# Optimization experiments

Measured on AMD Instinct MI355X. Metric: run time of the kernel, lower is better.

The kernel has to match this reference:

```python
import jax, jax.numpy as jnp
import numpy as np

N_BITS = 14
L = 1 << N_BITS
B, C_IN, C_OUT = 32, 32, 64

def _neigh_idx():
    # (L, n_bits): index j flipped at bit b -> j ^ (1<<b)
    s = jnp.arange(L)
    return jnp.stack([s ^ (1 << b) for b in range(N_BITS)], axis=1)

def setup_inputs() -> dict:
    key = jax.random.key(0)
    k1, k2, k3, k4 = jax.random.split(key, 4)
    x = jax.random.normal(k1, (B, C_IN, L), dtype=jnp.float32)
    w_self = jnp.ones((), dtype=jnp.float32)
    w_bits = jax.random.normal(k2, (N_BITS,), dtype=jnp.float32) * 0.1
    # Conv1d(kernel_size=1) weight squeezed to (C_out, C_in)
    mix_w = jax.random.normal(k3, (C_OUT, C_IN), dtype=jnp.float32) * (1.0 / np.sqrt(C_IN))
    mix_b = jax.random.normal(k4, (C_OUT,), dtype=jnp.float32) * 0.01
    return {"x": x, "w_self": w_self, "w_bits": w_bits, "mix_w": mix_w, "mix_b": mix_b}

def reference(x, w_self, w_bits, mix_w, mix_b):
    n_bits = w_bits.shape[0]
    idx = _neigh_idx()                          # (L, n_bits), int32
    xn = x[:, :, idx]                           # (B, C, L, n_bits) XOR-neighbor gather
    neigh_sum = jnp.einsum('bclk,k->bcl', xn, w_bits)
    y = w_self * x + neigh_sum
    y = y / (1.0 + n_bits)                      # agg == 'mean'
    # 1x1 conv mix: (B,C,L) x (C_out,C_in) -> (B,C_out,L)
    return jnp.einsum('bcl,oc->bol', y, mix_w) + mix_b[None, :, None]
```

## Files before the change

kernel.cpp:

```cpp
#include <hip/hip_runtime.h>

#define TILE  256
#define CIN   32
#define COUT  64
#define LSIZE 16384
#define NBITS 14

typedef float f32x4 __attribute__((ext_vector_type(4)));

__device__ __forceinline__ f32x4 splat4(float s) {
    f32x4 v = {s, s, s, s};
    return v;
}

__global__ __launch_bounds__(256, 5)
void hamming_fused(const float* __restrict__ x,
                   const float* __restrict__ w_self,
                   const float* __restrict__ w_bits,
                   const float* __restrict__ mix_w,
                   const float* __restrict__ mix_b,
                   float* __restrict__ out)
{
    __shared__ float xs[CIN][TILE];

    const int tid  = threadIdx.x;
    const int lane = tid & 63;
    const int wv   = tid >> 6;

    const int d    = blockIdx.x;
    const int xcd  = d & 7;
    const int j    = d >> 3;
    const int b    = xcd * 4 + (j >> 6);
    const int tile = j & 63;
    const int base = tile * TILE;
    const float* xb = x + (size_t)b * CIN * LSIZE;

    #pragma unroll
    for (int i = 0; i < 8; ++i) {
        const int r = wv + i * 4;
        const float* src = xb + (size_t)r * LSIZE + base + lane * 4;
        __builtin_amdgcn_global_load_lds(
            (const __attribute__((address_space(1))) void*)src,
            (__attribute__((address_space(3))) void*)&xs[r][lane * 4],
            16, 0, 0);
    }

    const float ws = w_self[0];
    float wb[NBITS];
    #pragma unroll
    for (int k = 0; k < NBITS; ++k) wb[k] = w_bits[k];

    __syncthreads();

    const int c0ch = wv * 8;
    const int colb = lane * 4;

    f32x4 yv[8];
    #pragma unroll
    for (int cc = 0; cc < 8; cc += 2) {
        f32x4 pf[2][6];
        #pragma unroll
        for (int u = 0; u < 2; ++u) {
            const float* xr = xb + (size_t)(c0ch + cc + u) * LSIZE;
            #pragma unroll
            for (int kk = 0; kk < 6; ++kk)
                pf[u][kk] = *(const f32x4*)(xr + ((base ^ (TILE << kk)) + colb));
        }
        #pragma unroll
        for (int u = 0; u < 2; ++u) {
            const int c = c0ch + cc + u;
            const f32x4 s = *(const f32x4*)&xs[c][colb];
            f32x4 a = s * ws;
            a.x += wb[0] * s.y; a.y += wb[0] * s.x; a.z += wb[0] * s.w; a.w += wb[0] * s.z;
            a.x += wb[1] * s.z; a.y += wb[1] * s.w; a.z += wb[1] * s.x; a.w += wb[1] * s.y;
            #pragma unroll
            for (int k = 2; k < 8; ++k) {
                const f32x4 t = *(const f32x4*)&xs[c][colb ^ (1 << k)];
                a += wb[k] * t;
            }
            #pragma unroll
            for (int kk = 0; kk < 6; ++kk)
                a += wb[8 + kk] * pf[u][kk];
            yv[cc + u] = a * (1.0f / 15.0f);
        }
    }
    __syncthreads();

    #pragma unroll
    for (int cc = 0; cc < 8; ++cc)
        *(f32x4*)&xs[c0ch + cc][colb] = yv[cc];
    __syncthreads();

    const int tx  = tid & 63;
    const int ty  = tid >> 6;
    const int cb2 = tx << 2;
    const int o0  = ty * 16;

    f32x4 acc[16];
    #pragma unroll
    for (int q = 0; q < 4; ++q) {
        const f32x4 b4 = *(const f32x4*)(mix_b + o0 + q * 4);
        acc[q * 4 + 0] = splat4(b4.x);
        acc[q * 4 + 1] = splat4(b4.y);
        acc[q * 4 + 2] = splat4(b4.z);
        acc[q * 4 + 3] = splat4(b4.w);
    }

    #pragma unroll 1
    for (int c0 = 0; c0 < CIN; c0 += 4) {
        const f32x4 y0 = *(const f32x4*)&xs[c0 + 0][cb2];
        const f32x4 y1 = *(const f32x4*)&xs[c0 + 1][cb2];
        const f32x4 y2 = *(const f32x4*)&xs[c0 + 2][cb2];
        const f32x4 y3 = *(const f32x4*)&xs[c0 + 3][cb2];
        const float* wp = mix_w + o0 * CIN + c0;
        #pragma unroll
        for (int jj = 0; jj < 16; ++jj) {
            const f32x4 w4 = *(const f32x4*)(wp + jj * CIN);
            acc[jj] += w4.x * y0;
            acc[jj] += w4.y * y1;
            acc[jj] += w4.z * y2;
            acc[jj] += w4.w * y3;
        }
    }

    float* ob = out + (size_t)b * COUT * LSIZE;
    #pragma unroll
    for (int jj = 0; jj < 16; ++jj) {
        f32x4* p = (f32x4*)(ob + (size_t)(o0 + jj) * LSIZE + base + cb2);
        __builtin_nontemporal_store(acc[jj], p);
    }
}

extern "C" void kernel_launch(void* const* d_in, const int* in_sizes, int n_in,
                              void* d_out, int out_size, void* d_ws, size_t ws_size,
                              hipStream_t stream) {
    const float* x      = (const float*)d_in[0];
    const float* w_self = (const float*)d_in[1];
    const float* w_bits = (const float*)d_in[2];
    const float* mix_w  = (const float*)d_in[3];
    const float* mix_b  = (const float*)d_in[4];
    float* out = (float*)d_out;

    hamming_fused<<<dim3(2048), 256, 0, stream>>>(x, w_self, w_bits, mix_w, mix_b, out);
}
```

Baseline: 232.9 us.

## Stage mix weights in LDS and software-pipeline neighbor prefetch across channels

Loads the 64x32 mix weight matrix into shared memory with async global-to-LDS copies, so the channel-mix loop reads weights from LDS instead of issuing scalar or global loads. The far-neighbor global prefetches become a rolling 3-slot pipeline issued two channels ahead, with the first two started before the LDS tile load. Results are written straight back into the shared tile, which drops one barrier and the yv register array. The mix loop is unrolled by 2 and the occupancy hint is lowered from 5 to 4 to allow more registers, at the cost of 8 KB extra LDS per block and possibly fewer resident waves.

Result: faster. 216.1 us (-7.2%).

```diff
diff --git a/kernel.cpp b/kernel.cpp
--- a/kernel.cpp
+++ b/kernel.cpp
@@ -13,7 +13,7 @@
     return v;
 }
 
-__global__ __launch_bounds__(256, 5)
+__global__ __launch_bounds__(256, 4)
 void hamming_fused(const float* __restrict__ x,
                    const float* __restrict__ w_self,
                    const float* __restrict__ w_bits,
@@ -22,6 +22,7 @@
                    float* __restrict__ out)
 {
     __shared__ float xs[CIN][TILE];
+    __shared__ float mwl[COUT * CIN];
 
     const int tid  = threadIdx.x;
     const int lane = tid & 63;
@@ -35,6 +36,18 @@
     const int base = tile * TILE;
     const float* xb = x + (size_t)b * CIN * LSIZE;
 
+    const int c0ch = wv * 8;
+    const int colb = lane * 4;
+
+    f32x4 pf[3][6];
+    #pragma unroll
+    for (int u = 0; u < 2; ++u) {
+        const float* xr = xb + (size_t)(c0ch + u) * LSIZE;
+        #pragma unroll
+        for (int kk = 0; kk < 6; ++kk)
+            pf[u][kk] = *(const f32x4*)(xr + ((base ^ (TILE << kk)) + colb));
+    }
+
     #pragma unroll
     for (int i = 0; i < 8; ++i) {
         const int r = wv + i * 4;
@@ -42,6 +55,15 @@
         __builtin_amdgcn_global_load_lds(
             (const __attribute__((address_space(1))) void*)src,
             (__attribute__((address_space(3))) void*)&xs[r][lane * 4],
+            16, 0, 0);
+    }
+    #pragma unroll
+    for (int i = 0; i < 2; ++i) {
+        const int q = tid + i * 256;
+        const float* src = mix_w + q * 4;
+        __builtin_amdgcn_global_load_lds(
+            (const __attribute__((address_space(1))) void*)src,
+            (__attribute__((address_space(3))) void*)&mwl[q * 4],
             16, 0, 0);
     }
 
@@ -52,43 +74,31 @@
 
     __syncthreads();
 
-    const int c0ch = wv * 8;
-    const int colb = lane * 4;
-
-    f32x4 yv[8];
     #pragma unroll
-    for (int cc = 0; cc < 8; cc += 2) {
-        f32x4 pf[2][6];
-        #pragma unroll
-        for (int u = 0; u < 2; ++u) {
-            const float* xr = xb + (size_t)(c0ch + cc + u) * LSIZE;
+    for (int cc = 0; cc < 8; ++cc) {
+        if (cc + 2 < 8) {
+            const float* xr = xb + (size_t)(c0ch + cc + 2) * LSIZE;
             #pragma unroll
             for (int kk = 0; kk < 6; ++kk)
-                pf[u][kk] = *(const f32x4*)(xr + ((base ^ (TILE << kk)) + colb));
+                pf[(cc + 2) % 3][kk] =
+                    *(const f32x4*)(xr + ((base ^ (TILE << kk)) + colb));
+        }
+        const int c = c0ch + cc;
+        const f32x4 s = *(const f32x4*)&xs[c][colb];
+        f32x4 a = s * ws;
+        a.x += wb[0] * s.y; a.y += wb[0] * s.x; a.z += wb[0] * s.w; a.w += wb[0] * s.z;
+        a.x += wb[1] * s.z; a.y += wb[1] * s.w; a.z += wb[1] * s.x; a.w += wb[1] * s.y;
+        #pragma unroll
+        for (int k = 2; k < 8; ++k) {
+            const f32x4 t = *(const f32x4*)&xs[c][colb ^ (1 << k)];
+            a += wb[k] * t;
         }
         #pragma unroll
-        for (int u = 0; u < 2; ++u) {
-            const int c = c0ch + cc + u;
-            const f32x4 s = *(const f32x4*)&xs[c][colb];
-            f32x4 a = s * ws;
-            a.x += wb[0] * s.y; a.y += wb[0] * s.x; a.z += wb[0] * s.w; a.w += wb[0] * s.z;
-            a.x += wb[1] * s.z; a.y += wb[1] * s.w; a.z += wb[1] * s.x; a.w += wb[1] * s.y;
-            #pragma unroll
-            for (int k = 2; k < 8; ++k) {
-                const f32x4 t = *(const f32x4*)&xs[c][colb ^ (1 << k)];
-                a += wb[k] * t;
-            }
-            #pragma unroll
-            for (int kk = 0; kk < 6; ++kk)
-                a += wb[8 + kk] * pf[u][kk];
-            yv[cc + u] = a * (1.0f / 15.0f);
-        }
+        for (int kk = 0; kk < 6; ++kk)
+            a += wb[8 + kk] * pf[cc % 3][kk];
+        a *= (1.0f / 15.0f);
+        *(f32x4*)&xs[c][colb] = a;
     }
-    __syncthreads();
-
-    #pragma unroll
-    for (int cc = 0; cc < 8; ++cc)
-        *(f32x4*)&xs[c0ch + cc][colb] = yv[cc];
     __syncthreads();
 
     const int tx  = tid & 63;
@@ -106,16 +116,15 @@
         acc[q * 4 + 3] = splat4(b4.w);
     }
 
-    #pragma unroll 1
+    #pragma unroll 2
     for (int c0 = 0; c0 < CIN; c0 += 4) {
         const f32x4 y0 = *(const f32x4*)&xs[c0 + 0][cb2];
         const f32x4 y1 = *(const f32x4*)&xs[c0 + 1][cb2];
         const f32x4 y2 = *(const f32x4*)&xs[c0 + 2][cb2];
         const f32x4 y3 = *(const f32x4*)&xs[c0 + 3][cb2];
-        const float* wp = mix_w + o0 * CIN + c0;
         #pragma unroll
         for (int jj = 0; jj < 16; ++jj) {
-            const f32x4 w4 = *(const f32x4*)(wp + jj * CIN);
+            const f32x4 w4 = *(const f32x4*)&mwl[(o0 + jj) * CIN + c0];
             acc[jj] += w4.x * y0;
             acc[jj] += w4.y * y1;
             acc[jj] += w4.z * y2;
```
